# Kernel tuning notes

Hardware: AMD Instinct MI355X
Metric: run time of the kernel (lower is better)

## Reference

```python
import jax, jax.numpy as jnp
import numpy as np
from jax.scipy.special import logsumexp

B, F, V, C, K, KP = 8192, 32, 64, 32, 8, 7  # batch, features, values/feature, classes, gate options, padded pair candidates
TEMP = 1.0
EPS = 1e-06


def _structure():
    # candidate 0 = self table; candidates 1..7 = pair tables conditioned on preceding features
    mask = np.zeros((F - 1, K), dtype=bool)
    mask[:, 0] = True
    cond = np.zeros((F - 1, KP), dtype=np.int32)
    for i in range(F - 1):
        fi = i + 1
        for j in range(min(fi, KP)):
            mask[i, j + 1] = True
            cond[i, j] = fi - 1 - j
    return jnp.asarray(cond), jnp.asarray(mask)


def setup_inputs() -> dict:
    key = jax.random.key(0)
    ks = jax.random.split(key, 6)
    cond_index, valid_mask = _structure()
    return {
        "x": jax.random.randint(ks[0], (B, F), 0, V, dtype=jnp.int32),
        "training": True,
        "class_logits": jax.random.normal(ks[1], (C,), jnp.float32) * 0.1,
        "table0": jax.random.normal(ks[2], (V, C), jnp.float32) * 0.1,
        "self_tables": jax.random.normal(ks[3], (F - 1, V, C), jnp.float32) * 0.1,
        "pair_tables": jax.random.normal(ks[4], (F - 1, KP, V, V, C), jnp.float32) * 0.1,
        "structure_logits": jax.random.normal(ks[5], (F - 1, K), jnp.float32) * 0.1,
        "u_noise": jax.random.uniform(jax.random.fold_in(key, 7), (F - 1, K), jnp.float32),
        "cond_index": cond_index,
        "valid_mask": valid_mask,
    }


def reference(x, training, class_logits, table0, self_tables, pair_tables,
              structure_logits, u_noise, cond_index, valid_mask):
    # class prior term
    cl = class_logits - logsumexp(class_logits)  # [C]
    t0 = table0 - logsumexp(table0, axis=0, keepdims=True)  # [V,C]
    out = cl[None, :] + t0[x[:, 0]]  # [B,C]

    # Gumbel-softmax gate over candidate parent sets (training path)
    g = -jnp.log(-jnp.log(u_noise + EPS) + EPS)
    gate_logits = jnp.where(valid_mask, (structure_logits + g) / TEMP, -jnp.inf)
    w = jax.nn.softmax(gate_logits, axis=-1)  # [F-1,K]; padded entries get weight 0

    f_idx = jnp.arange(F - 1)
    xs = x[:, 1:]  # [B,F-1] feature values

    # self (class-only) candidate tables, normalized over the feature-value axis
    st = self_tables - logsumexp(self_tables, axis=1, keepdims=True)  # [F-1,V,C]
    self_g = st[f_idx[None, :], xs]  # [B,F-1,C]
    out = out + jnp.einsum('bfc,f->bc', self_g, w[:, 0])

    # pair candidate tables, normalized over the feature-value axis (axis 2)
    pt = pair_tables - logsumexp(pair_tables, axis=2, keepdims=True)  # [F-1,KP,V,V,C]
    xc = x[:, cond_index]  # [B,F-1,KP] conditioning feature values
    k_idx = jnp.arange(KP)
    pair_g = pt[f_idx[None, :, None], k_idx[None, None, :], xs[:, :, None], xc]  # [B,F-1,KP,C]
    out = out + jnp.einsum('bfkc,fk->bc', pair_g, w[:, 1:])
    return out
```

## Files before the change

### kernel.cpp

```cpp
#include <hip/hip_runtime.h>
#include <math.h>

#define B_  8192
#define F_  32
#define V_  64
#define C_  32
#define KP_ 7
#define EPS_ 1e-6f

#define WS_OFF  256
#define WS_ETAB 288
#define WS_G    512
#define WS_LSE  66048
#define LSE_BANK4 111104

__device__ const int d_split[9] = {0, 25, 50, 74, 99, 123, 148, 172, 196};

__global__ __launch_bounds__(256)
void lse_prep_kernel(const float* __restrict__ pt,
                     const float* __restrict__ cl, const float* __restrict__ t0,
                     const float* __restrict__ st, const float* __restrict__ sl,
                     const float* __restrict__ un, float* __restrict__ ws) {
    if (blockIdx.x < 434) {
        int fk   = blockIdx.x >> 1;
        int half = blockIdx.x & 1;
        int t    = threadIdx.x;
        const float4* __restrict__ p =
            (const float4*)(pt + (size_t)fk * (V_ * V_ * C_)
                               + (size_t)half * 32 * (V_ * C_));
        const float4* p0 = p + t;
        const float4* p1 = p + 256 + t;
        float4 s0 = make_float4(0.f, 0.f, 0.f, 0.f);
        float4 s1 = make_float4(0.f, 0.f, 0.f, 0.f);
        #pragma unroll 4
        for (int a = 0; a < 32; a++) {
            float4 l0 = p0[a * 512];
            float4 l1 = p1[a * 512];
            s0.x += __expf(l0.x); s0.y += __expf(l0.y);
            s0.z += __expf(l0.z); s0.w += __expf(l0.w);
            s1.x += __expf(l1.x); s1.y += __expf(l1.y);
            s1.z += __expf(l1.z); s1.w += __expf(l1.w);
        }
        float4* lseP = (float4*)(ws + WS_LSE) + (size_t)half * LSE_BANK4;
        lseP[fk * 512 + t]       = s0;
        lseP[fk * 512 + 256 + t] = s1;
    } else {
        __shared__ float gl[31][8];
        __shared__ float wsm[31][8];
        __shared__ float lsf[31][32];
        int tid = threadIdx.x;
        if (tid < 248) {
            int f = tid >> 3, k = tid & 7;
            int kmax = min(f + 1, KP_);
            bool valid = (k <= kmax);
            float u = un[tid];
            float g = -__logf(-__logf(u + EPS_) + EPS_);
            gl[f][k] = valid ? (sl[tid] + g) : -INFINITY;
        } else {
            ws[tid] = 0.f;
        }
        if (tid < 200) {
            int q = tid / 25, i = tid % 25;
            int g = d_split[q] + i;
            int packed;
            if (g < d_split[q + 1]) {
                int f = 0, base = 0;
                for (;;) { int cnt = min(f + 1, KP_); if (g < base + cnt) break; base += cnt; f++; }
                int k = g - base;
                packed = ((f * 8 + k + 1) << 20) | ((f * KP_ + k) << 12) | ((f + 1) << 6) | (f - k);
            } else {
                packed = (248 << 20);
            }
            ((int*)ws)[WS_ETAB + tid] = packed;
        }
        __syncthreads();
        if (tid < 248) {
            int f = tid >> 3, k = tid & 7;
            float m = -INFINITY;
            #pragma unroll
            for (int j = 0; j < 8; j++) m = fmaxf(m, gl[f][j]);
            float s = 0.f;
            #pragma unroll
            for (int j = 0; j < 8; j++) s += __expf(gl[f][j] - m);
            float wv = __expf(gl[f][k] - m) / s;
            wsm[f][k] = wv;
            ws[tid] = wv;
        }
        for (int i = tid; i < 992; i += 256) {
            int f = i >> 5, c = i & 31;
            float s = 0.f;
            #pragma unroll 8
            for (int v = 0; v < V_; v++) s += __expf(st[(f * V_ + v) * C_ + c]);
            lsf[f][c] = __logf(s);
        }
        __syncthreads();
        if (tid < 32) {
            int c = tid;
            float scl = 0.f;
            #pragma unroll
            for (int j = 0; j < C_; j++) scl += __expf(cl[j]);
            float lse_cl = __logf(scl);
            float s0 = 0.f;
            #pragma unroll 8
            for (int v = 0; v < V_; v++) s0 += __expf(t0[v * C_ + c]);
            float lse_t0 = __logf(s0);
            float acc = cl[c] - lse_cl - lse_t0;
            for (int f = 0; f < 31; f++) acc -= wsm[f][0] * lsf[f][c];
            ws[WS_OFF + c] = acc;
        }
    }
}

__global__ __launch_bounds__(256)
void foldg_kernel(const float* __restrict__ t0, const float* __restrict__ st,
                  float* __restrict__ ws) {
    int idx = blockIdx.x * 256 + threadIdx.x;
    int c4 = idx & 7, v = (idx >> 3) & 63, j = idx >> 9;
    int nk = min(KP_, 31 - j);
    const float4* lse4 = (const float4*)(ws + WS_LSE);
    float4 g;
    if (j == 0) {
        g = ((const float4*)t0)[v * 8 + c4];
    } else {
        float w0 = ws[(j - 1) * 8];
        float4 sv = ((const float4*)st)[((j - 1) * V_ + v) * 8 + c4];
        g.x = w0 * sv.x; g.y = w0 * sv.y; g.z = w0 * sv.z; g.w = w0 * sv.w;
    }
    for (int k = 0; k < nk; k++) {
        int f = j + k;
        float wv = ws[f * 8 + k + 1];
        int iq = ((f * KP_ + k) * V_ + v) * 8 + c4;
        float4 sa = lse4[iq];
        float4 sb = lse4[LSE_BANK4 + iq];
        g.x -= wv * __logf(sa.x + sb.x);
        g.y -= wv * __logf(sa.y + sb.y);
        g.z -= wv * __logf(sa.z + sb.z);
        g.w -= wv * __logf(sa.w + sb.w);
    }
    ((float4*)(ws + WS_G))[idx] = g;
}

__global__ __launch_bounds__(256)
void main_kernel(const int* __restrict__ x, const float* __restrict__ pt,
                 const float* __restrict__ ws, float* __restrict__ out) {
    __shared__ int   xsh[4 * 33];
    __shared__ float wsh[256];
    __shared__ int   etab[200];
    __shared__ float4 offv[8];
    __shared__ float4 part[7][32];
    int tid = threadIdx.x;
    if (tid < 128) xsh[(tid >> 5) * 33 + (tid & 31)] = x[blockIdx.x * 128 + tid];
    wsh[tid] = ws[tid];
    if (tid < 200) etab[tid] = ((const int*)ws)[WS_ETAB + tid];
    if (tid < 8)   offv[tid] = ((const float4*)(ws + WS_OFF))[tid];
    __syncthreads();

    const float4* __restrict__ G4 = (const float4*)(ws + WS_G);
    int q  = tid >> 5;
    int r  = (tid >> 3) & 3;
    int c4 = tid & 7;
    const int* xrow = &xsh[r * 33];
    float4 acc = make_float4(0.f, 0.f, 0.f, 0.f);

    #pragma unroll
    for (int jj = 0; jj < 4; jj++) {
        int j = q * 4 + jj;
        float4 gv = G4[(j * V_ + xrow[j]) * 8 + c4];
        acc.x += gv.x; acc.y += gv.y; acc.z += gv.z; acc.w += gv.w;
    }
    if (q == 0) {
        float4 ov = offv[c4];
        acc.x += ov.x; acc.y += ov.y; acc.z += ov.z; acc.w += ov.w;
    }

    int beg = q * 25;
    #pragma unroll
    for (int ch = 0; ch < 5; ch++) {
        float4 pv[5];
        float  wt[5];
        #pragma unroll
        for (int i = 0; i < 5; i++) {
            int pk = etab[beg + ch * 5 + i];
            int ci = pk & 63, fi = (pk >> 6) & 63;
            int fk = (pk >> 12) & 255, widx = (pk >> 20) & 255;
            int xv = xrow[fi], xc = xrow[ci];
            pv[i] = *(const float4*)(pt + ((size_t)(fk * V_ + xv) * V_ + xc) * C_ + c4 * 4);
            wt[i] = wsh[widx];
        }
        #pragma unroll
        for (int i = 0; i < 5; i++) {
            acc.x += wt[i] * pv[i].x; acc.y += wt[i] * pv[i].y;
            acc.z += wt[i] * pv[i].z; acc.w += wt[i] * pv[i].w;
        }
    }

    if (q > 0) part[q - 1][r * 8 + c4] = acc;
    __syncthreads();
    if (q == 0) {
        #pragma unroll
        for (int p = 0; p < 7; p++) {
            float4 pv = part[p][r * 8 + c4];
            acc.x += pv.x; acc.y += pv.y; acc.z += pv.z; acc.w += pv.w;
        }
        ((float4*)out)[(blockIdx.x * 4 + r) * 8 + c4] = acc;
    }
}

extern "C" void kernel_launch(void* const* d_in, const int* in_sizes, int n_in,
                              void* d_out, int out_size, void* d_ws, size_t ws_size,
                              hipStream_t stream) {
    const int*   x   = (const int*)  d_in[0];
    const float* cl  = (const float*)d_in[2];
    const float* t0  = (const float*)d_in[3];
    const float* st  = (const float*)d_in[4];
    const float* pt  = (const float*)d_in[5];
    const float* sl  = (const float*)d_in[6];
    const float* un  = (const float*)d_in[7];
    float* ws  = (float*)d_ws;
    float* out = (float*)d_out;

    lse_prep_kernel<<<435, 256, 0, stream>>>(pt, cl, t0, st, sl, un, ws);
    foldg_kernel<<<64, 256, 0, stream>>>(t0, st, ws);
    main_kernel<<<2048, 256, 0, stream>>>(x, pt, ws, out);
}
```

Measured before the change: 233.6 us.

## Fuse pair-table gather with LSE reduction and split G gather into final kernel

The pair-table gather, which needs only the gate weights and raw pair tables, now runs in the same launch as the pair-table logsumexp reduction, so the two heavy memory passes can overlap on the GPU. Each gather block recomputes the Gumbel-softmax weights and the entry table locally instead of waiting on a prep kernel. A lightweight final kernel adds the folded G-table terms and the offset to the staged partial results. The LSE reduction is also split four ways across 868 blocks for more parallelism. The cost is an extra partial-result buffer round trip through global memory and redundant per-block gate computation.

Result: faster. 223.7 us (-4.2%).

```diff
diff --git a/kernel.cpp b/kernel.cpp
--- a/kernel.cpp
+++ b/kernel.cpp
@@ -9,31 +9,34 @@
 #define EPS_ 1e-6f
 
 #define WS_OFF  256
-#define WS_ETAB 288
 #define WS_G    512
 #define WS_LSE  66048
 #define LSE_BANK4 111104
+#define WS_PART 1843712
+
+#define NBLK_LSE 868
+#define NBLK_PAIR 2048
 
 __device__ const int d_split[9] = {0, 25, 50, 74, 99, 123, 148, 172, 196};
 
 __global__ __launch_bounds__(256)
-void lse_prep_kernel(const float* __restrict__ pt,
-                     const float* __restrict__ cl, const float* __restrict__ t0,
-                     const float* __restrict__ st, const float* __restrict__ sl,
-                     const float* __restrict__ un, float* __restrict__ ws) {
-    if (blockIdx.x < 434) {
-        int fk   = blockIdx.x >> 1;
-        int half = blockIdx.x & 1;
-        int t    = threadIdx.x;
+void fused_kernel(const int* __restrict__ x, const float* __restrict__ pt,
+                  const float* __restrict__ cl, const float* __restrict__ t0,
+                  const float* __restrict__ st, const float* __restrict__ sl,
+                  const float* __restrict__ un, float* __restrict__ ws) {
+    if (blockIdx.x < NBLK_LSE) {
+        int fk = blockIdx.x >> 2;
+        int qa = blockIdx.x & 3;
+        int t  = threadIdx.x;
         const float4* __restrict__ p =
             (const float4*)(pt + (size_t)fk * (V_ * V_ * C_)
-                               + (size_t)half * 32 * (V_ * C_));
+                               + (size_t)qa * 16 * (V_ * C_));
         const float4* p0 = p + t;
         const float4* p1 = p + 256 + t;
         float4 s0 = make_float4(0.f, 0.f, 0.f, 0.f);
         float4 s1 = make_float4(0.f, 0.f, 0.f, 0.f);
         #pragma unroll 4
-        for (int a = 0; a < 32; a++) {
+        for (int a = 0; a < 16; a++) {
             float4 l0 = p0[a * 512];
             float4 l1 = p1[a * 512];
             s0.x += __expf(l0.x); s0.y += __expf(l0.y);
@@ -41,10 +44,10 @@
             s1.x += __expf(l1.x); s1.y += __expf(l1.y);
             s1.z += __expf(l1.z); s1.w += __expf(l1.w);
         }
-        float4* lseP = (float4*)(ws + WS_LSE) + (size_t)half * LSE_BANK4;
+        float4* lseP = (float4*)(ws + WS_LSE) + (size_t)qa * LSE_BANK4;
         lseP[fk * 512 + t]       = s0;
         lseP[fk * 512 + 256 + t] = s1;
-    } else {
+    } else if (blockIdx.x == NBLK_LSE) {
         __shared__ float gl[31][8];
         __shared__ float wsm[31][8];
         __shared__ float lsf[31][32];
@@ -58,6 +61,58 @@
             gl[f][k] = valid ? (sl[tid] + g) : -INFINITY;
         } else {
             ws[tid] = 0.f;
+        }
+        __syncthreads();
+        if (tid < 248) {
+            int f = tid >> 3, k = tid & 7;
+            float m = -INFINITY;
+            #pragma unroll
+            for (int j = 0; j < 8; j++) m = fmaxf(m, gl[f][j]);
+            float s = 0.f;
+            #pragma unroll
+            for (int j = 0; j < 8; j++) s += __expf(gl[f][j] - m);
+            float wv = __expf(gl[f][k] - m) / s;
+            wsm[f][k] = wv;
+            ws[tid] = wv;
+        }
+        for (int i = tid; i < 992; i += 256) {
+            int f = i >> 5, c = i & 31;
+            float s = 0.f;
+            #pragma unroll 8
+            for (int v = 0; v < V_; v++) s += __expf(st[(f * V_ + v) * C_ + c]);
+            lsf[f][c] = __logf(s);
+        }
+        __syncthreads();
+        if (tid < 32) {
+            int c = tid;
+            float scl = 0.f;
+            #pragma unroll
+            for (int j = 0; j < C_; j++) scl += __expf(cl[j]);
+            float lse_cl = __logf(scl);
+            float s0 = 0.f;
+            #pragma unroll 8
+            for (int v = 0; v < V_; v++) s0 += __expf(t0[v * C_ + c]);
+            float lse_t0 = __logf(s0);
+            float acc = cl[c] - lse_cl - lse_t0;
+            for (int f = 0; f < 31; f++) acc -= wsm[f][0] * lsf[f][c];
+            ws[WS_OFF + c] = acc;
+        }
+    } else {
+        __shared__ int    xsh[4 * 33];
+        __shared__ float  wsh[256];
+        __shared__ int    etab[200];
+        __shared__ float4 part[7][32];
+        __shared__ float  gl[31][8];
+        int tid = threadIdx.x;
+        int pb  = blockIdx.x - (NBLK_LSE + 1);
+        if (tid < 128) xsh[(tid >> 5) * 33 + (tid & 31)] = x[pb * 128 + tid];
+        if (tid < 248) {
+            int f = tid >> 3, k = tid & 7;
+            int kmax = min(f + 1, KP_);
+            bool valid = (k <= kmax);
+            float u = un[tid];
+            float g = -__logf(-__logf(u + EPS_) + EPS_);
+            gl[f][k] = valid ? (sl[tid] + g) : -INFINITY;
         }
         if (tid < 200) {
             int q = tid / 25, i = tid % 25;
@@ -71,42 +126,60 @@
             } else {
                 packed = (248 << 20);
             }
-            ((int*)ws)[WS_ETAB + tid] = packed;
-        }
-        __syncthreads();
-        if (tid < 248) {
-            int f = tid >> 3, k = tid & 7;
+            etab[tid] = packed;
+        }
+        __syncthreads();
+        if (tid < 248) {
+            int f = tid >> 3;
             float m = -INFINITY;
             #pragma unroll
             for (int j = 0; j < 8; j++) m = fmaxf(m, gl[f][j]);
             float s = 0.f;
             #pragma unroll
             for (int j = 0; j < 8; j++) s += __expf(gl[f][j] - m);
-            float wv = __expf(gl[f][k] - m) / s;
-            wsm[f][k] = wv;
-            ws[tid] = wv;
-        }
-        for (int i = tid; i < 992; i += 256) {
-            int f = i >> 5, c = i & 31;
-            float s = 0.f;
-            #pragma unroll 8
-            for (int v = 0; v < V_; v++) s += __expf(st[(f * V_ + v) * C_ + c]);
-            lsf[f][c] = __logf(s);
-        }
-        __syncthreads();
-        if (tid < 32) {
-            int c = tid;
-            float scl = 0.f;
-            #pragma unroll
-            for (int j = 0; j < C_; j++) scl += __expf(cl[j]);
-            float lse_cl = __logf(scl);
-            float s0 = 0.f;
-            #pragma unroll 8
-            for (int v = 0; v < V_; v++) s0 += __expf(t0[v * C_ + c]);
-            float lse_t0 = __logf(s0);
-            float acc = cl[c] - lse_cl - lse_t0;
-            for (int f = 0; f < 31; f++) acc -= wsm[f][0] * lsf[f][c];
-            ws[WS_OFF + c] = acc;
+            wsh[tid] = __expf(gl[f][tid & 7] - m) / s;
+        } else {
+            wsh[tid] = 0.f;
+        }
+        __syncthreads();
+
+        int q  = tid >> 5;
+        int r  = (tid >> 3) & 3;
+        int c4 = tid & 7;
+        const int* xrow = &xsh[r * 33];
+        const float* __restrict__ ptb = pt + c4 * 4;
+        float4 acc = make_float4(0.f, 0.f, 0.f, 0.f);
+
+        int beg = q * 25;
+        #pragma unroll
+        for (int ch = 0; ch < 5; ch++) {
+            float4 pv[5];
+            float  wt[5];
+            #pragma unroll
+            for (int i = 0; i < 5; i++) {
+                int pk = etab[beg + ch * 5 + i];
+                int ci = pk & 63, fi = (pk >> 6) & 63;
+                int fk = (pk >> 12) & 255, widx = (pk >> 20) & 255;
+                int xv = xrow[fi], xc = xrow[ci];
+                pv[i] = *(const float4*)(ptb + ((size_t)(fk * V_ + xv) * V_ + xc) * C_);
+                wt[i] = wsh[widx];
+            }
+            #pragma unroll
+            for (int i = 0; i < 5; i++) {
+                acc.x += wt[i] * pv[i].x; acc.y += wt[i] * pv[i].y;
+                acc.z += wt[i] * pv[i].z; acc.w += wt[i] * pv[i].w;
+            }
+        }
+
+        if (q > 0) part[q - 1][r * 8 + c4] = acc;
+        __syncthreads();
+        if (q == 0) {
+            #pragma unroll
+            for (int p = 0; p < 7; p++) {
+                float4 pv2 = part[p][r * 8 + c4];
+                acc.x += pv2.x; acc.y += pv2.y; acc.z += pv2.z; acc.w += pv2.w;
+            }
+            ((float4*)(ws + WS_PART))[(pb * 4 + r) * 8 + c4] = acc;
         }
     }
 }
@@ -131,79 +204,41 @@
         float wv = ws[f * 8 + k + 1];
         int iq = ((f * KP_ + k) * V_ + v) * 8 + c4;
         float4 sa = lse4[iq];
-        float4 sb = lse4[LSE_BANK4 + iq];
-        g.x -= wv * __logf(sa.x + sb.x);
-        g.y -= wv * __logf(sa.y + sb.y);
-        g.z -= wv * __logf(sa.z + sb.z);
-        g.w -= wv * __logf(sa.w + sb.w);
+        float4 sb = lse4[1 * LSE_BANK4 + iq];
+        float4 sc = lse4[2 * LSE_BANK4 + iq];
+        float4 sd = lse4[3 * LSE_BANK4 + iq];
+        g.x -= wv * __logf(sa.x + sb.x + sc.x + sd.x);
+        g.y -= wv * __logf(sa.y + sb.y + sc.y + sd.y);
+        g.z -= wv * __logf(sa.z + sb.z + sc.z + sd.z);
+        g.w -= wv * __logf(sa.w + sb.w + sc.w + sd.w);
     }
     ((float4*)(ws + WS_G))[idx] = g;
 }
 
 __global__ __launch_bounds__(256)
-void main_kernel(const int* __restrict__ x, const float* __restrict__ pt,
-                 const float* __restrict__ ws, float* __restrict__ out) {
-    __shared__ int   xsh[4 * 33];
-    __shared__ float wsh[256];
-    __shared__ int   etab[200];
+void maing_kernel(const int* __restrict__ x, const float* __restrict__ ws,
+                  float* __restrict__ out) {
+    __shared__ int    xsh[32][33];
     __shared__ float4 offv[8];
-    __shared__ float4 part[7][32];
     int tid = threadIdx.x;
-    if (tid < 128) xsh[(tid >> 5) * 33 + (tid & 31)] = x[blockIdx.x * 128 + tid];
-    wsh[tid] = ws[tid];
-    if (tid < 200) etab[tid] = ((const int*)ws)[WS_ETAB + tid];
-    if (tid < 8)   offv[tid] = ((const float4*)(ws + WS_OFF))[tid];
+    int rbase = blockIdx.x * 32;
+    for (int i = tid; i < 1024; i += 256) {
+        int rr = i >> 5, jj = i & 31;
+        xsh[rr][jj] = x[(rbase + rr) * 32 + jj];
+    }
+    if (tid < 8) offv[tid] = ((const float4*)(ws + WS_OFF))[tid];
     __syncthreads();
-
+    int r = tid >> 3, c4 = tid & 7;
     const float4* __restrict__ G4 = (const float4*)(ws + WS_G);
-    int q  = tid >> 5;
-    int r  = (tid >> 3) & 3;
-    int c4 = tid & 7;
-    const int* xrow = &xsh[r * 33];
-    float4 acc = make_float4(0.f, 0.f, 0.f, 0.f);
-
-    #pragma unroll
-    for (int jj = 0; jj < 4; jj++) {
-        int j = q * 4 + jj;
-        float4 gv = G4[(j * V_ + xrow[j]) * 8 + c4];
+    float4 acc = ((const float4*)(ws + WS_PART))[(rbase + r) * 8 + c4];
+    float4 ov = offv[c4];
+    acc.x += ov.x; acc.y += ov.y; acc.z += ov.z; acc.w += ov.w;
+    #pragma unroll 8
+    for (int j = 0; j < 32; j++) {
+        float4 gv = G4[(j * V_ + xsh[r][j]) * 8 + c4];
         acc.x += gv.x; acc.y += gv.y; acc.z += gv.z; acc.w += gv.w;
     }
-    if (q == 0) {
-        float4 ov = offv[c4];
-        acc.x += ov.x; acc.y += ov.y; acc.z += ov.z; acc.w += ov.w;
-    }
-
-    int beg = q * 25;
-    #pragma unroll
-    for (int ch = 0; ch < 5; ch++) {
-        float4 pv[5];
-        float  wt[5];
-        #pragma unroll
-        for (int i = 0; i < 5; i++) {
-            int pk = etab[beg + ch * 5 + i];
-            int ci = pk & 63, fi = (pk >> 6) & 63;
-            int fk = (pk >> 12) & 255, widx = (pk >> 20) & 255;
-            int xv = xrow[fi], xc = xrow[ci];
-            pv[i] = *(const float4*)(pt + ((size_t)(fk * V_ + xv) * V_ + xc) * C_ + c4 * 4);
-            wt[i] = wsh[widx];
-        }
-        #pragma unroll
-        for (int i = 0; i < 5; i++) {
-            acc.x += wt[i] * pv[i].x; acc.y += wt[i] * pv[i].y;
-            acc.z += wt[i] * pv[i].z; acc.w += wt[i] * pv[i].w;
-        }
-    }
-
-    if (q > 0) part[q - 1][r * 8 + c4] = acc;
-    __syncthreads();
-    if (q == 0) {
-        #pragma unroll
-        for (int p = 0; p < 7; p++) {
-            float4 pv = part[p][r * 8 + c4];
-            acc.x += pv.x; acc.y += pv.y; acc.z += pv.z; acc.w += pv.w;
-        }
-        ((float4*)out)[(blockIdx.x * 4 + r) * 8 + c4] = acc;
-    }
+    ((float4*)out)[(rbase + r) * 8 + c4] = acc;
 }
 
 extern "C" void kernel_launch(void* const* d_in, const int* in_sizes, int n_in,
@@ -219,7 +254,7 @@
     float* ws  = (float*)d_ws;
     float* out = (float*)d_out;
 
-    lse_prep_kernel<<<435, 256, 0, stream>>>(pt, cl, t0, st, sl, un, ws);
+    fused_kernel<<<NBLK_LSE + 1 + NBLK_PAIR, 256, 0, stream>>>(x, pt, cl, t0, st, sl, un, ws);
     foldg_kernel<<<64, 256, 0, stream>>>(t0, st, ws);
-    main_kernel<<<2048, 256, 0, stream>>>(x, pt, ws, out);
-}
+    maing_kernel<<<256, 256, 0, stream>>>(x, ws, out);
+}
```
